# Kernel tuning notes

Measured on AMD Instinct MI355X. Metric: run time of the kernel, lower is better.

The kernel has to match this reference:

```python
import jax, jax.numpy as jnp
import numpy as np

N = 8192       # patients (nodes)
E = 262144     # edges per graph (avg degree 32)
DF = 128       # dim_final
SLOPE = 0.25   # leaky_relu negative slope


def _spmm(rows, cols, vals, dense):
    # out[i] = sum_{e: rows[e]==i} vals[e] * dense[cols[e]]  == sparse_adj @ dense
    return jax.ops.segment_sum(vals[:, None] * dense[cols], rows, num_segments=N)


def _branch(x, rows, cols, vals, w1, b1, w2, b2):
    # GraphGCN: gc1 -> leaky_relu -> (dropout: identity in eval) -> gc2 -> leaky_relu
    h = _spmm(rows, cols, vals, x @ w1) + b1
    h = jax.nn.leaky_relu(h, negative_slope=SLOPE)
    h = _spmm(rows, cols, vals, h @ w2) + b2
    return jax.nn.leaky_relu(h, negative_slope=SLOPE)


def setup_inputs() -> dict:
    key = jax.random.key(0)
    ks = jax.random.split(key, 40)
    i = 0

    def xav(k, shape):
        std = (2.0 / (shape[0] + shape[1])) ** 0.5
        return std * jax.random.normal(k, shape, dtype=jnp.float32)

    inp = {}
    feat_dims = {"RNAseq": 4096, "dnam": 4096, "cn": 4096, "mic": 1024}
    for name, d in feat_dims.items():
        inp[name] = jax.random.normal(ks[i], (N, d), dtype=jnp.float32); i += 1
    for g in range(1, 5):
        inp[f"rows{g}"] = jax.random.randint(ks[i], (E,), 0, N, dtype=jnp.int32); i += 1
        inp[f"cols{g}"] = jax.random.randint(ks[i], (E,), 0, N, dtype=jnp.int32); i += 1
        inp[f"vals{g}"] = jax.random.uniform(ks[i], (E,), dtype=jnp.float32); i += 1
    # per-branch params: (in_dim, hid_dim); suffixes r=RNAseq, d=meth, c=CN, m=miRNA
    specs = {"r": (4096, 512), "d": (4096, 512), "c": (4096, 512), "m": (1024, 256)}
    for s, (din, dh) in specs.items():
        inp[f"w1_{s}"] = xav(ks[i], (din, dh)); i += 1
        inp[f"b1_{s}"] = jnp.zeros((dh,), jnp.float32)
        inp[f"w2_{s}"] = xav(ks[i], (dh, DF)); i += 1
        inp[f"b2_{s}"] = jnp.zeros((DF,), jnp.float32)
    return inp


def reference(RNAseq, dnam, cn, mic,
              rows1, cols1, vals1, rows2, cols2, vals2,
              rows3, cols3, vals3, rows4, cols4, vals4,
              w1_r, b1_r, w2_r, b2_r,
              w1_d, b1_d, w2_d, b2_d,
              w1_c, b1_c, w2_c, b2_c,
              w1_m, b1_m, w2_m, b2_m):
    x_r = _branch(RNAseq, rows1, cols1, vals1, w1_r, b1_r, w2_r, b2_r)
    x_d = _branch(dnam,   rows2, cols2, vals2, w1_d, b1_d, w2_d, b2_d)
    x_c = _branch(cn,     rows3, cols3, vals3, w1_c, b1_c, w2_c, b2_c)
    x_m = _branch(mic,    rows4, cols4, vals4, w1_m, b1_m, w2_m, b2_m)
    return (x_r + x_d + x_c + x_m) / 4.0
```

## Files before the change

### kernel.cpp

```cpp
#include <hip/hip_runtime.h>

#define N_NODES 8192
#define N_EDGES 262144
#define SLOPE 0.25f

typedef __attribute__((ext_vector_type(8))) short bf16x8;
typedef __attribute__((ext_vector_type(4))) float f32x4;

__device__ __forceinline__ float lrelu(float x) { return x >= 0.f ? x : SLOPE * x; }

__device__ __forceinline__ unsigned short bf16_rne(float x) {
    unsigned u = __float_as_uint(x);
    return (unsigned short)((u + 0x7FFFu + ((u >> 16) & 1u)) >> 16);
}
__device__ __forceinline__ float bf2f(unsigned short h) {
    return __uint_as_float(((unsigned)h) << 16);
}
__device__ __forceinline__ unsigned packtr(float a, float b) {
    return __builtin_amdgcn_perm(__float_as_uint(b), __float_as_uint(a), 0x07060302u);
}
__device__ __forceinline__ bf16x8 pack8t(const float4& a, const float4& b) {
    union { unsigned u[4]; bf16x8 v; } r;
    r.u[0] = packtr(a.x, a.y);
    r.u[1] = packtr(a.z, a.w);
    r.u[2] = packtr(b.x, b.y);
    r.u[3] = packtr(b.z, b.w);
    return r.v;
}

#define GLDS16(g, l)                                                              \
    __builtin_amdgcn_global_load_lds((const __attribute__((address_space(1))) void*)(g), \
                                     (__attribute__((address_space(3))) void*)(l), 16, 0, 0)

struct TransB8 { const float* W[8]; unsigned short* Th[8]; int K[8]; int N[8]; };

__global__ __launch_bounds__(256) void tsplit8(TransB8 tb) {
    const int z = blockIdx.z;
    const int K = tb.K[z], N = tb.N[z];
    const int k0 = blockIdx.x * 32, n0 = blockIdx.y * 32;
    if (k0 >= K || n0 >= N) return;
    __shared__ float t[32][33];
    const int tx = threadIdx.x & 31, ty = threadIdx.x >> 5;
    const float* W = tb.W[z];
#pragma unroll
    for (int i = 0; i < 32; i += 8)
        t[ty + i][tx] = W[(size_t)(k0 + ty + i) * N + n0 + tx];
    __syncthreads();
#pragma unroll
    for (int i = 0; i < 32; i += 8) {
        const int n = ty + i;
        tb.Th[z][(size_t)(n0 + n) * K + k0 + tx] = bf16_rne(t[tx][n]);
    }
}

struct GemmB {
    const void* A[4];
    const unsigned short* Bh[4];
    unsigned short* C[4];
    int K[4];
    int NT[4];
};

template <int NF, int AF32>
__global__ __launch_bounds__(256, 2) void gemm_bf16s(GemmB gb) {
    constexpr int BGR = NF / 2;
    const int nwg = gridDim.x * gridDim.y * gridDim.z;
    int id = (blockIdx.z * gridDim.y + blockIdx.y) * gridDim.x + blockIdx.x;
    const int cpx = nwg >> 3;
    id = (id & 7) * cpx + (id >> 3);
    const int by = id % gridDim.y;
    const int rest = id / gridDim.y;
    const int bx = rest % gridDim.x;
    const int z = rest / gridDim.x;

    const int nt = gb.NT[z];
    if (by >= nt) return;
    const int K = gb.K[z];
    const int N = nt * (NF * 32);
    const float* __restrict__ Af = (const float*)gb.A[z];
    const unsigned short* __restrict__ Ab = (const unsigned short*)gb.A[z];
    const unsigned short* __restrict__ Bh = gb.Bh[z];
    unsigned short* __restrict__ C = gb.C[z];

    __shared__ unsigned short As[3 * 4096];
    __shared__ unsigned short Bs[3 * NF * 1024];
    const int tid = threadIdx.x;
    const int w = tid >> 6, lane = tid & 63;
    const int wm = w >> 1, wn = w & 1;
    const int bm0 = bx * 128, bn0 = by * (NF * 32);

    auto stageB = [&](int buf, int kt) {
        const int k0 = kt << 5;
#pragma unroll
        for (int i = 0; i < BGR; ++i) {
            const int f = (w * BGR + i) * 64 + lane;
            const int row = f >> 2, s = f & 3;
            const int kg = s ^ ((row >> 1) & 3);
            GLDS16(Bh + (size_t)(bn0 + row) * K + k0 + kg * 8,
                   &Bs[buf * (NF * 1024) + (w * BGR + i) * 512]);
        }
    };
    auto stageAglds = [&](int buf, int kt) {
        const int k0 = kt << 5;
#pragma unroll
        for (int i = 0; i < 2; ++i) {
            const int f = (w * 2 + i) * 64 + lane;
            const int row = f >> 2, s = f & 3;
            const int kg = s ^ ((row >> 1) & 3);
            GLDS16(Ab + (size_t)(bm0 + row) * K + k0 + kg * 8,
                   &As[buf * 4096 + (w * 2 + i) * 512]);
        }
    };
    auto issueA = [&](float4 (&ar)[2][2], int kt) {
        const int k0 = kt << 5;
#pragma unroll
        for (int i = 0; i < 2; ++i) {
            const int f = i * 256 + tid;
            const int row = f >> 2, s = f & 3;
            const int kg = s ^ ((row >> 1) & 3);
            const float* src = Af + (size_t)(bm0 + row) * K + k0 + kg * 8;
            ar[i][0] = *reinterpret_cast<const float4*>(src);
            ar[i][1] = *reinterpret_cast<const float4*>(src + 4);
        }
    };
    auto writeA = [&](float4 (&ar)[2][2], int buf) {
#pragma unroll
        for (int i = 0; i < 2; ++i)
            *reinterpret_cast<bf16x8*>(&As[buf * 4096 + (i * 256 + tid) * 8]) =
                pack8t(ar[i][0], ar[i][1]);
    };

    f32x4 acc[4][NF];
#pragma unroll
    for (int mf = 0; mf < 4; ++mf)
#pragma unroll
        for (int nf = 0; nf < NF; ++nf) acc[mf][nf] = (f32x4){0.f, 0.f, 0.f, 0.f};

    const int nk = K >> 5;
    float4 aE[2][2], aO[2][2];

    if constexpr (AF32) {
        issueA(aE, 0); stageB(0, 0);
        issueA(aO, 1); stageB(1, 1);
        asm volatile("s_waitcnt vmcnt(12)" ::: "memory");
        writeA(aE, 0);
        asm volatile("s_waitcnt lgkmcnt(0)" ::: "memory");
    } else {
        stageAglds(0, 0); stageB(0, 0);
        stageAglds(1, 1); stageB(1, 1);
    }

    auto body = [&](int t, float4 (&iset)[2][2], float4 (&wset)[2][2]) {
        const int cb = t % 3;
        if (t + 2 < nk) {
            if constexpr (AF32) issueA(iset, t + 2);
            else stageAglds((t + 2) % 3, t + 2);
            stageB((t + 2) % 3, t + 2);
            if constexpr (AF32) asm volatile("s_waitcnt vmcnt(16)" ::: "memory");
            else asm volatile("s_waitcnt vmcnt(8)" ::: "memory");
        } else if (t + 1 < nk) {
            if constexpr (AF32) asm volatile("s_waitcnt vmcnt(8)" ::: "memory");
            else asm volatile("s_waitcnt vmcnt(4)" ::: "memory");
        } else {
            asm volatile("s_waitcnt vmcnt(0)" ::: "memory");
        }
        __builtin_amdgcn_s_barrier();
        __builtin_amdgcn_sched_barrier(0);

        const int kq = lane >> 4;
        bf16x8 a[4], b[NF];
#pragma unroll
        for (int mf = 0; mf < 4; ++mf) {
            const int r = wm * 64 + mf * 16 + (lane & 15);
            a[mf] = *reinterpret_cast<const bf16x8*>(
                &As[cb * 4096 + r * 32 + ((kq ^ ((r >> 1) & 3)) << 3)]);
        }
#pragma unroll
        for (int nf = 0; nf < NF; ++nf) {
            const int r = wn * (NF * 16) + nf * 16 + (lane & 15);
            b[nf] = *reinterpret_cast<const bf16x8*>(
                &Bs[cb * (NF * 1024) + r * 32 + ((kq ^ ((r >> 1) & 3)) << 3)]);
        }

        if constexpr (AF32) {
            if (t + 1 < nk) {
                if (t + 2 < nk) asm volatile("s_waitcnt vmcnt(12)" ::: "memory");
                else asm volatile("s_waitcnt vmcnt(4)" ::: "memory");
                writeA(wset, (t + 1) % 3);
            }
        }

        __builtin_amdgcn_s_setprio(1);
#pragma unroll
        for (int mf = 0; mf < 4; ++mf)
#pragma unroll
            for (int nf = 0; nf < NF; ++nf)
                acc[mf][nf] = __builtin_amdgcn_mfma_f32_16x16x32_bf16(a[mf], b[nf], acc[mf][nf], 0, 0, 0);
        __builtin_amdgcn_s_setprio(0);

        asm volatile("s_waitcnt lgkmcnt(0)" ::: "memory");
        __builtin_amdgcn_s_barrier();
    };

    for (int t = 0; t < nk; t += 2) {
        body(t, aE, aO);
        body(t + 1, aO, aE);
    }

    const int cr = (lane >> 4) * 4, cc = lane & 15;
#pragma unroll
    for (int mf = 0; mf < 4; ++mf)
#pragma unroll
        for (int nf = 0; nf < NF; ++nf)
#pragma unroll
            for (int j = 0; j < 4; ++j)
                C[(size_t)(bm0 + wm * 64 + mf * 16 + cr + j) * N + bn0 + wn * (NF * 16) + nf * 16 + cc] =
                    bf16_rne(acc[mf][nf][j]);
}

struct GraphPtrs {
    const int* r[4];
    const int* c[4];
    const float* v[4];
};

__global__ __launch_bounds__(256) void hist4(GraphPtrs p, int* __restrict__ cnt4) {
    const int g = blockIdx.y;
    const int e = blockIdx.x * 256 + threadIdx.x;
    atomicAdd(&cnt4[g * N_NODES + p.r[g][e]], 1);
}

__global__ __launch_bounds__(256) void scan4(const int* __restrict__ cnt4,
                                             int* __restrict__ rs4,
                                             int* __restrict__ cur4) {
    const int g = blockIdx.x;
    const int* cnt = cnt4 + g * N_NODES;
    int* row_start = rs4 + (size_t)g * (N_NODES + 1);
    int* cursor = cur4 + g * N_NODES;
    __shared__ int ssum[256];
    const int t = threadIdx.x;
    int local[32];
    int s = 0;
#pragma unroll
    for (int j = 0; j < 32; ++j) { local[j] = cnt[t * 32 + j]; s += local[j]; }
    ssum[t] = s;
    __syncthreads();
    for (int off = 1; off < 256; off <<= 1) {
        const int v = ssum[t];
        const int add = (t >= off) ? ssum[t - off] : 0;
        __syncthreads();
        ssum[t] = v + add;
        __syncthreads();
    }
    int run = (t == 0) ? 0 : ssum[t - 1];
#pragma unroll
    for (int j = 0; j < 32; ++j) {
        row_start[t * 32 + j] = run;
        cursor[t * 32 + j] = run;
        run += local[j];
    }
    if (t == 255) row_start[N_NODES] = run;
}

__global__ __launch_bounds__(256) void scatter4(GraphPtrs p, int* __restrict__ cur4,
                                                unsigned long long* __restrict__ pe4) {
    const int g = blockIdx.y;
    const int e = blockIdx.x * 256 + threadIdx.x;
    const int r = p.r[g][e];
    const int pos = atomicAdd(&cur4[g * N_NODES + r], 1);
    pe4[(size_t)g * N_EDGES + pos] =
        (unsigned long long)(unsigned)p.c[g][e] |
        ((unsigned long long)__float_as_uint(p.v[g][e]) << 32);
}

struct SpmmB {
    const int* rs[4];
    const unsigned long long* pe[4];
    const unsigned short* Y[4];
    const float* bi[4];
    unsigned short* H[4];
    int nc[4];
};

__global__ __launch_bounds__(256) void spmm_h1x(SpmmB sb) {
    const int id = blockIdx.x;
    const int xcd = id & 7;
    const int z = xcd >> 1;
    const int rb = ((id >> 3) << 1) + (id & 1);
    const int row = rb * 4 + (threadIdx.x >> 6);
    const int lane = threadIdx.x & 63;
    const int nc = sb.nc[z];
    const int* rs = sb.rs[z];
    const int s = rs[row], e1 = rs[row + 1];
    const unsigned long long* pe = sb.pe[z];
    const unsigned short* Y = sb.Y[z];
    const float* bi = sb.bi[z];

    if (nc == 512) {
        const int base = lane * 8;
        float acc[8];
#pragma unroll
        for (int j = 0; j < 8; ++j) acc[j] = 0.f;
        for (int e = s; e < e1; ++e) {
            const unsigned long long ev = pe[e];
            const float v = __uint_as_float((unsigned)(ev >> 32));
            const bf16x8 raw = *reinterpret_cast<const bf16x8*>(
                Y + (size_t)(unsigned)ev * 512 + base);
#pragma unroll
            for (int j = 0; j < 8; ++j)
                acc[j] = fmaf(v, bf2f((unsigned short)raw[j]), acc[j]);
        }
        bf16x8 vh;
#pragma unroll
        for (int j = 0; j < 8; ++j) vh[j] = (short)bf16_rne(lrelu(acc[j] + bi[base + j]));
        *reinterpret_cast<bf16x8*>(sb.H[z] + (size_t)row * 512 + base) = vh;
    } else {
        const int base = lane * 4;
        float acc[4];
#pragma unroll
        for (int j = 0; j < 4; ++j) acc[j] = 0.f;
        for (int e = s; e < e1; ++e) {
            const unsigned long long ev = pe[e];
            const float v = __uint_as_float((unsigned)(ev >> 32));
            const ushort4 raw = *reinterpret_cast<const ushort4*>(
                Y + (size_t)(unsigned)ev * 256 + base);
            acc[0] = fmaf(v, bf2f(raw.x), acc[0]);
            acc[1] = fmaf(v, bf2f(raw.y), acc[1]);
            acc[2] = fmaf(v, bf2f(raw.z), acc[2]);
            acc[3] = fmaf(v, bf2f(raw.w), acc[3]);
        }
        ushort4 vh;
        vh.x = bf16_rne(lrelu(acc[0] + bi[base + 0]));
        vh.y = bf16_rne(lrelu(acc[1] + bi[base + 1]));
        vh.z = bf16_rne(lrelu(acc[2] + bi[base + 2]));
        vh.w = bf16_rne(lrelu(acc[3] + bi[base + 3]));
        *reinterpret_cast<ushort4*>(sb.H[z] + (size_t)row * 256 + base) = vh;
    }
}

template <int NC>
__global__ __launch_bounds__(256) void spmm_h1(const int* __restrict__ rs,
                                               const unsigned long long* __restrict__ pe,
                                               const unsigned short* __restrict__ Y,
                                               const float* __restrict__ bi,
                                               unsigned short* __restrict__ Hd) {
    constexpr int PL = NC / 64;
    const int row = (blockIdx.x * 256 + threadIdx.x) >> 6;
    const int lane = threadIdx.x & 63;
    const int s = rs[row], e1 = rs[row + 1];
    const int base = lane * PL;
    float acc[PL];
#pragma unroll
    for (int j = 0; j < PL; ++j) acc[j] = 0.f;
    for (int e = s; e < e1; ++e) {
        const unsigned long long ev = pe[e];
        const float v = __uint_as_float((unsigned)(ev >> 32));
        const unsigned short* y = Y + (size_t)(unsigned)ev * NC + base;
        if constexpr (PL == 8) {
            const bf16x8 raw = *reinterpret_cast<const bf16x8*>(y);
#pragma unroll
            for (int j = 0; j < 8; ++j)
                acc[j] = fmaf(v, bf2f((unsigned short)raw[j]), acc[j]);
        } else {
            const ushort4 raw = *reinterpret_cast<const ushort4*>(y);
            acc[0] = fmaf(v, bf2f(raw.x), acc[0]);
            acc[1] = fmaf(v, bf2f(raw.y), acc[1]);
            acc[2] = fmaf(v, bf2f(raw.z), acc[2]);
            acc[3] = fmaf(v, bf2f(raw.w), acc[3]);
        }
    }
    unsigned short* H = Hd + (size_t)row * NC + base;
    if constexpr (PL == 8) {
        bf16x8 vh;
#pragma unroll
        for (int j = 0; j < 8; ++j) vh[j] = (short)bf16_rne(lrelu(acc[j] + bi[base + j]));
        *reinterpret_cast<bf16x8*>(H) = vh;
    } else {
        ushort4 vh;
        vh.x = bf16_rne(lrelu(acc[0] + bi[base + 0]));
        vh.y = bf16_rne(lrelu(acc[1] + bi[base + 1]));
        vh.z = bf16_rne(lrelu(acc[2] + bi[base + 2]));
        vh.w = bf16_rne(lrelu(acc[3] + bi[base + 3]));
        *reinterpret_cast<ushort4*>(H) = vh;
    }
}

struct Out4 { const float* b2[4]; };

__global__ __launch_bounds__(256) void spmm_out4(const int* __restrict__ rs4,
                                                 const unsigned long long* __restrict__ pe4,
                                                 const unsigned short* __restrict__ Y2all,
                                                 Out4 ob, float* __restrict__ out) {
    const int row = (blockIdx.x * 256 + threadIdx.x) >> 6;
    const int lane = threadIdx.x & 63;
    const int base = lane * 2;
    float r0 = 0.f, r1 = 0.f;
#pragma unroll
    for (int b = 0; b < 4; ++b) {
        const int* rs = rs4 + (size_t)b * (N_NODES + 1);
        const int s = rs[row], e1 = rs[row + 1];
        const unsigned long long* pe = pe4 + (size_t)b * N_EDGES;
        const unsigned short* Y = Y2all + (size_t)b * N_NODES * 128;
        float a0 = 0.f, a1 = 0.f;
        for (int e = s; e < e1; ++e) {
            const unsigned long long ev = pe[e];
            const float v = __uint_as_float((unsigned)(ev >> 32));
            const unsigned u = *reinterpret_cast<const unsigned*>(
                Y + (size_t)(unsigned)ev * 128 + base);
            a0 = fmaf(v, __uint_as_float(u << 16), a0);
            a1 = fmaf(v, __uint_as_float(u & 0xFFFF0000u), a1);
        }
        const float* bi = ob.b2[b];
        r0 += lrelu(a0 + bi[base]);
        r1 += lrelu(a1 + bi[base + 1]);
    }
    *reinterpret_cast<float2*>(out + (size_t)row * 128 + base) =
        make_float2(0.25f * r0, 0.25f * r1);
}

__global__ __launch_bounds__(256) void spmm_out1(const int* __restrict__ rs,
                                                 const unsigned long long* __restrict__ pe,
                                                 const unsigned short* __restrict__ Y,
                                                 const float* __restrict__ bias,
                                                 float* __restrict__ out, int first) {
    const int row = (blockIdx.x * 256 + threadIdx.x) >> 6;
    const int lane = threadIdx.x & 63;
    const int base = lane * 2;
    const int s = rs[row], e1 = rs[row + 1];
    float a0 = 0.f, a1 = 0.f;
    for (int e = s; e < e1; ++e) {
        const unsigned long long ev = pe[e];
        const float v = __uint_as_float((unsigned)(ev >> 32));
        const unsigned u = *reinterpret_cast<const unsigned*>(
            Y + (size_t)(unsigned)ev * 128 + base);
        a0 = fmaf(v, __uint_as_float(u << 16), a0);
        a1 = fmaf(v, __uint_as_float(u & 0xFFFF0000u), a1);
    }
    float r0 = 0.25f * lrelu(a0 + bias[base]);
    float r1 = 0.25f * lrelu(a1 + bias[base + 1]);
    float* o = out + (size_t)row * 128 + base;
    if (!first) {
        const float2 p = *reinterpret_cast<const float2*>(o);
        r0 += p.x;
        r1 += p.y;
    }
    *reinterpret_cast<float2*>(o) = make_float2(r0, r1);
}

extern "C" void kernel_launch(void* const* d_in, const int* in_sizes, int n_in,
                              void* d_out, int out_size, void* d_ws, size_t ws_size,
                              hipStream_t stream) {
    const float* X[4] = {(const float*)d_in[0], (const float*)d_in[1],
                         (const float*)d_in[2], (const float*)d_in[3]};
    GraphPtrs gp;
    for (int b = 0; b < 4; ++b) {
        gp.r[b] = (const int*)d_in[4 + 3 * b];
        gp.c[b] = (const int*)d_in[5 + 3 * b];
        gp.v[b] = (const float*)d_in[6 + 3 * b];
    }
    const float *w1[4], *b1[4], *w2[4], *b2[4];
    for (int b = 0; b < 4; ++b) {
        w1[b] = (const float*)d_in[16 + 4 * b + 0];
        b1[b] = (const float*)d_in[16 + 4 * b + 1];
        w2[b] = (const float*)d_in[16 + 4 * b + 2];
        b2[b] = (const float*)d_in[16 + 4 * b + 3];
    }
    const int din[4] = {4096, 4096, 4096, 1024};
    const int dh[4] = {512, 512, 512, 256};
    float* out = (float*)d_out;

    char* wsc = (char*)d_ws;
    size_t off = 0;
    auto carve = [&](size_t bytes) {
        void* p = wsc + off;
        off += (bytes + 255) & ~(size_t)255;
        return p;
    };
    int* cnt4 = (int*)carve((size_t)4 * N_NODES * 4);
    int* rs4 = (int*)carve((size_t)4 * (N_NODES + 1) * 4);
    int* cur4 = (int*)carve((size_t)4 * N_NODES * 4);
    unsigned long long* pe4 = (unsigned long long*)carve((size_t)4 * N_EDGES * 8);

    size_t tier1_base = off;
    unsigned short *W1h[4], *W2h[4], *Y1[4], *H1[4];
    for (int b = 0; b < 4; ++b) W1h[b] = (unsigned short*)carve((size_t)dh[b] * din[b] * 2);
    for (int b = 0; b < 4; ++b) W2h[b] = (unsigned short*)carve((size_t)128 * dh[b] * 2);
    for (int b = 0; b < 4; ++b) Y1[b] = (unsigned short*)carve((size_t)N_NODES * dh[b] * 2);
    for (int b = 0; b < 4; ++b) H1[b] = (unsigned short*)carve((size_t)N_NODES * dh[b] * 2);
    unsigned short* Y2all = (unsigned short*)carve((size_t)4 * N_NODES * 128 * 2);
    const bool tier1 = (off <= ws_size);
    unsigned short* Y2s[4];
    if (tier1) {
        for (int b = 0; b < 4; ++b) Y2s[b] = Y2all + (size_t)b * N_NODES * 128;
    } else {
        off = tier1_base;
        unsigned short* w1h = (unsigned short*)carve((size_t)512 * 4096 * 2);
        unsigned short* w2h = (unsigned short*)carve((size_t)128 * 512 * 2);
        unsigned short* y1 = (unsigned short*)carve((size_t)N_NODES * 512 * 2);
        unsigned short* h1 = (unsigned short*)carve((size_t)N_NODES * 512 * 2);
        unsigned short* y2 = (unsigned short*)carve((size_t)N_NODES * 128 * 2);
        for (int b = 0; b < 4; ++b) {
            W1h[b] = w1h; W2h[b] = w2h;
            Y1[b] = y1; H1[b] = h1; Y2s[b] = y2;
        }
    }

    hipMemsetAsync(cnt4, 0, (size_t)4 * N_NODES * sizeof(int), stream);
    {
        dim3 g(N_EDGES / 256, 4);
        hist4<<<g, 256, 0, stream>>>(gp, cnt4);
        scan4<<<4, 256, 0, stream>>>(cnt4, rs4, cur4);
        scatter4<<<g, 256, 0, stream>>>(gp, cur4, pe4);
    }

    if (tier1) {
        TransB8 tt;
        for (int b = 0; b < 4; ++b) {
            tt.W[b] = w1[b]; tt.Th[b] = W1h[b]; tt.K[b] = din[b]; tt.N[b] = dh[b];
            tt.W[4 + b] = w2[b]; tt.Th[4 + b] = W2h[b]; tt.K[4 + b] = dh[b]; tt.N[4 + b] = 128;
        }
        tsplit8<<<dim3(128, 16, 8), 256, 0, stream>>>(tt);

        GemmB g1;
        for (int b = 0; b < 4; ++b) {
            g1.A[b] = X[b]; g1.Bh[b] = W1h[b];
            g1.C[b] = Y1[b]; g1.K[b] = din[b]; g1.NT[b] = dh[b] / 256;
        }
        gemm_bf16s<8, 1><<<dim3(64, 2, 4), 256, 0, stream>>>(g1);

        SpmmB s1;
        for (int b = 0; b < 4; ++b) {
            s1.rs[b] = rs4 + (size_t)b * (N_NODES + 1);
            s1.pe[b] = pe4 + (size_t)b * N_EDGES;
            s1.Y[b] = Y1[b]; s1.bi[b] = b1[b]; s1.H[b] = H1[b];
            s1.nc[b] = dh[b];
        }
        spmm_h1x<<<8192, 256, 0, stream>>>(s1);

        GemmB g2;
        for (int b = 0; b < 4; ++b) {
            g2.A[b] = H1[b]; g2.Bh[b] = W2h[b];
            g2.C[b] = Y2s[b]; g2.K[b] = dh[b]; g2.NT[b] = 1;
        }
        gemm_bf16s<4, 0><<<dim3(64, 1, 4), 256, 0, stream>>>(g2);

        Out4 ob;
        for (int b = 0; b < 4; ++b) ob.b2[b] = b2[b];
        spmm_out4<<<N_NODES / 4, 256, 0, stream>>>(rs4, pe4, Y2all, ob, out);
    } else {
        for (int b = 0; b < 4; ++b) {
            TransB8 tt;
            tt.W[0] = w1[b]; tt.Th[0] = W1h[b]; tt.K[0] = din[b]; tt.N[0] = dh[b];
            tsplit8<<<dim3(din[b] / 32, dh[b] / 32, 1), 256, 0, stream>>>(tt);
            GemmB g1;
            g1.A[0] = X[b]; g1.Bh[0] = W1h[b];
            g1.C[0] = Y1[b]; g1.K[0] = din[b]; g1.NT[0] = dh[b] / 256;
            gemm_bf16s<8, 1><<<dim3(64, dh[b] / 256 ? dh[b] / 256 : 1, 1), 256, 0, stream>>>(g1);
            if (dh[b] == 512)
                spmm_h1<512><<<N_NODES / 4, 256, 0, stream>>>(
                    rs4 + (size_t)b * (N_NODES + 1), pe4 + (size_t)b * N_EDGES,
                    Y1[b], b1[b], H1[b]);
            else
                spmm_h1<256><<<N_NODES / 4, 256, 0, stream>>>(
                    rs4 + (size_t)b * (N_NODES + 1), pe4 + (size_t)b * N_EDGES,
                    Y1[b], b1[b], H1[b]);
            TransB8 t2;
            t2.W[0] = w2[b]; t2.Th[0] = W2h[b]; t2.K[0] = dh[b]; t2.N[0] = 128;
            tsplit8<<<dim3(dh[b] / 32, 4, 1), 256, 0, stream>>>(t2);
            GemmB g2;
            g2.A[0] = H1[b]; g2.Bh[0] = W2h[b];
            g2.C[0] = Y2s[b]; g2.K[0] = dh[b]; g2.NT[0] = 1;
            gemm_bf16s<4, 0><<<dim3(64, 1, 1), 256, 0, stream>>>(g2);
            spmm_out1<<<N_NODES / 4, 256, 0, stream>>>(
                rs4 + (size_t)b * (N_NODES + 1), pe4 + (size_t)b * N_EDGES,
                Y2s[b], b2[b], out, b == 0);
        }
    }
}
```

Measured before the change: 529.3 us.

## Add 256x256-tile 8-wave ping-pong GEMM for first-layer projection

Adds a new GEMM kernel with 512 threads per block and 256x256 output tiles that splits each 64-wide K step into eight phases. In each phase, global loads for the next tile (fp32 A converted to bf16 through registers, bf16 B via direct-to-LDS loads) interleave with MFMA compute, using explicit waitcnt, barriers and setprio. It replaces the 128-row-tile gemm_bf16s for the large X@W1 products, aiming to halve A/B reloads across tiles and overlap memory with compute. The cost is higher register and LDS pressure with one block per CU, fragile hand-counted vmcnt waits, and half as many blocks.

```diff
diff --git a/kernel.cpp b/kernel.cpp
--- a/kernel.cpp
+++ b/kernel.cpp
@@ -60,6 +60,169 @@
     int K[4];
     int NT[4];
 };
+
+__global__ __launch_bounds__(512, 1) void gemm8p(GemmB gb) {
+    const int nwg = gridDim.x * gridDim.y * gridDim.z;
+    int id = (blockIdx.z * gridDim.y + blockIdx.y) * gridDim.x + blockIdx.x;
+    const int cpx = nwg >> 3;
+    id = (id & 7) * cpx + (id >> 3);
+    const int by = id % gridDim.y;
+    const int rest = id / gridDim.y;
+    const int bx = rest % gridDim.x;
+    const int z = rest / gridDim.x;
+    if (by >= gb.NT[z]) return;
+
+    const int K = gb.K[z];
+    const int N = gb.NT[z] * 256;
+    const float* __restrict__ Af = (const float*)gb.A[z];
+    const unsigned short* __restrict__ Bh = gb.Bh[z];
+    unsigned short* __restrict__ C = gb.C[z];
+    const int bm0 = bx * 256, bn0 = by * 256;
+
+    __shared__ unsigned short As[2 * 16384];
+    __shared__ unsigned short Bs[2 * 16384];
+
+    const int tid = threadIdx.x;
+    const int w = tid >> 6, lane = tid & 63;
+    const int wm = w >> 2, wn = w & 3;
+    const int m15 = lane & 15, kq = lane >> 4;
+    const int arow = tid >> 2;
+    const int aslot = (tid & 3) * 2;
+
+    float4 S0[4], S1[4];
+
+    auto issueA = [&](float4 (&S)[4], int kt, int h) {
+        const float* src = Af + (size_t)(bm0 + h * 128 + arow) * K + kt * 64 + aslot * 8;
+        S[0] = *reinterpret_cast<const float4*>(src);
+        S[1] = *reinterpret_cast<const float4*>(src + 4);
+        S[2] = *reinterpret_cast<const float4*>(src + 8);
+        S[3] = *reinterpret_cast<const float4*>(src + 12);
+    };
+    auto writeA = [&](float4 (&S)[4], int kt, int h) {
+        const int buf = kt & 1;
+        const int r2 = h * 128 + arow;
+        unsigned short* base = As + buf * 16384 + r2 * 64;
+        const int sw = r2 & 7;
+        *reinterpret_cast<bf16x8*>(base + ((aslot ^ sw) * 8)) = pack8t(S[0], S[1]);
+        *reinterpret_cast<bf16x8*>(base + (((aslot + 1) ^ sw) * 8)) = pack8t(S[2], S[3]);
+    };
+    auto stageB = [&](int kt, int h) {
+        const int buf = kt & 1;
+#pragma unroll
+        for (int j = 0; j < 2; ++j) {
+            const int g = j * 512 + tid;
+            const int row = g >> 3;
+            const int sl = (g & 7) ^ (row & 7);
+            GLDS16(Bh + (size_t)(bn0 + h * 128 + row) * K + kt * 64 + sl * 8,
+                   &Bs[buf * 16384 + h * 8192 + (j * 512 + w * 64) * 8]);
+        }
+    };
+
+    f32x4 acc[8][4];
+#pragma unroll
+    for (int mf = 0; mf < 8; ++mf)
+#pragma unroll
+        for (int nf = 0; nf < 4; ++nf) acc[mf][nf] = (f32x4){0.f, 0.f, 0.f, 0.f};
+
+    const int nT = K >> 6;
+    const int nI = nT >> 1;
+
+    issueA(S0, 0, 0); stageB(0, 0);
+    issueA(S1, 0, 1); stageB(0, 1);
+    asm volatile("s_waitcnt vmcnt(0)" ::: "memory");
+    writeA(S0, 0, 0);
+    writeA(S1, 0, 1);
+    issueA(S1, 1, 0); stageB(1, 0);
+    asm volatile("s_waitcnt lgkmcnt(0)" ::: "memory");
+    __builtin_amdgcn_sched_barrier(0);
+    __builtin_amdgcn_s_barrier();
+
+#define PHASE(TAU, MH, NH, STAGE_BLOCK)                                                   \
+    {                                                                                     \
+        bf16x8 afr[4][2], bfr[2][2];                                                      \
+        _Pragma("unroll") for (int j = 0; j < 4; ++j) {                                   \
+            const int rA = wm * 128 + (MH * 4 + j) * 16 + m15;                            \
+            const int swz = rA & 7;                                                       \
+            afr[j][0] = *reinterpret_cast<const bf16x8*>(                                 \
+                &As[TAU * 16384 + rA * 64 + ((kq ^ swz) * 8)]);                           \
+            afr[j][1] = *reinterpret_cast<const bf16x8*>(                                 \
+                &As[TAU * 16384 + rA * 64 + (((4 + kq) ^ swz) * 8)]);                     \
+        }                                                                                 \
+        _Pragma("unroll") for (int n = 0; n < 2; ++n) {                                   \
+            const int rB = wn * 64 + (NH * 2 + n) * 16 + m15;                             \
+            const int swz = rB & 7;                                                       \
+            bfr[n][0] = *reinterpret_cast<const bf16x8*>(                                 \
+                &Bs[TAU * 16384 + rB * 64 + ((kq ^ swz) * 8)]);                           \
+            bfr[n][1] = *reinterpret_cast<const bf16x8*>(                                 \
+                &Bs[TAU * 16384 + rB * 64 + (((4 + kq) ^ swz) * 8)]);                     \
+        }                                                                                 \
+        STAGE_BLOCK                                                                       \
+        __builtin_amdgcn_s_barrier();                                                     \
+        asm volatile("s_waitcnt lgkmcnt(0)" ::: "memory");                                \
+        __builtin_amdgcn_sched_barrier(0);                                                \
+        __builtin_amdgcn_s_setprio(1);                                                    \
+        _Pragma("unroll") for (int j = 0; j < 4; ++j)                                     \
+            _Pragma("unroll") for (int n = 0; n < 2; ++n) {                               \
+                acc[MH * 4 + j][NH * 2 + n] = __builtin_amdgcn_mfma_f32_16x16x32_bf16(    \
+                    afr[j][0], bfr[n][0], acc[MH * 4 + j][NH * 2 + n], 0, 0, 0);          \
+                acc[MH * 4 + j][NH * 2 + n] = __builtin_amdgcn_mfma_f32_16x16x32_bf16(    \
+                    afr[j][1], bfr[n][1], acc[MH * 4 + j][NH * 2 + n], 0, 0, 0);          \
+            }                                                                             \
+        __builtin_amdgcn_s_setprio(0);                                                    \
+        __builtin_amdgcn_s_barrier();                                                     \
+    }
+
+    for (int i = 0; i < nI; ++i) {
+        const int t1 = 2 * i + 1, n0 = 2 * i + 2, n1 = 2 * i + 3;
+        const bool lastI = (i == nI - 1);
+
+        PHASE(0, 0, 0, {
+            issueA(S0, t1, 1);
+            asm volatile("s_waitcnt vmcnt(6)" ::: "memory");
+            writeA(S1, t1, 0);
+        })
+        PHASE(0, 0, 1, { stageB(t1, 1); })
+        PHASE(0, 1, 0, {
+            if (!lastI) {
+                issueA(S1, n0, 0);
+                asm volatile("s_waitcnt vmcnt(6)" ::: "memory");
+            } else {
+                asm volatile("s_waitcnt vmcnt(2)" ::: "memory");
+            }
+            writeA(S0, t1, 1);
+        })
+        PHASE(0, 1, 1, { if (!lastI) stageB(n0, 0); })
+        PHASE(1, 0, 0, {
+            if (!lastI) {
+                issueA(S0, n0, 1);
+                asm volatile("s_waitcnt vmcnt(6)" ::: "memory");
+                writeA(S1, n0, 0);
+            } else {
+                asm volatile("s_waitcnt vmcnt(0)" ::: "memory");
+            }
+        })
+        PHASE(1, 0, 1, { if (!lastI) stageB(n0, 1); })
+        PHASE(1, 1, 0, {
+            if (!lastI) {
+                issueA(S1, n1, 0);
+                asm volatile("s_waitcnt vmcnt(6)" ::: "memory");
+                writeA(S0, n0, 1);
+            }
+        })
+        PHASE(1, 1, 1, { if (!lastI) stageB(n1, 0); })
+    }
+#undef PHASE
+
+    const int cr = kq * 4;
+#pragma unroll
+    for (int mf = 0; mf < 8; ++mf)
+#pragma unroll
+        for (int nf = 0; nf < 4; ++nf)
+#pragma unroll
+            for (int j = 0; j < 4; ++j)
+                C[(size_t)(bm0 + wm * 128 + mf * 16 + cr + j) * N + bn0 + wn * 64 + nf * 16 + m15] =
+                    bf16_rne(acc[mf][nf][j]);
+}
 
 template <int NF, int AF32>
 __global__ __launch_bounds__(256, 2) void gemm_bf16s(GemmB gb) {
@@ -526,7 +689,7 @@
             g1.A[b] = X[b]; g1.Bh[b] = W1h[b];
             g1.C[b] = Y1[b]; g1.K[b] = din[b]; g1.NT[b] = dh[b] / 256;
         }
-        gemm_bf16s<8, 1><<<dim3(64, 2, 4), 256, 0, stream>>>(g1);
+        gemm8p<<<dim3(32, 2, 4), 512, 0, stream>>>(g1);
 
         SpmmB s1;
         for (int b = 0; b < 4; ++b) {
```

After: 537.4 us. About the same (+1.5%).
